# Kernel tuning notes

Measured on AMD Instinct MI355X. Metric: run time of the kernel, lower is better.

Reference implementation:

```python
import jax, jax.numpy as jnp
import numpy as np
import math

N_HEAD = 16

def setup_inputs() -> dict:
    key = jax.random.key(0)
    ks = jax.random.split(key, 5)
    B, T, C = 4, 2048, 1024
    x = jax.random.normal(ks[0], (B, T, C), dtype=jnp.float32)
    # xavier-uniform-ish scale for dense kernels
    W_attn = jax.random.normal(ks[1], (C, 3 * C), dtype=jnp.float32) * (1.0 / math.sqrt(C))
    b_attn = jnp.zeros((3 * C,), dtype=jnp.float32)
    W_proj = jax.random.normal(ks[2], (C, C), dtype=jnp.float32) * (1.0 / math.sqrt(C))
    b_proj = jnp.zeros((C,), dtype=jnp.float32)
    return {"x": x, "W_attn": W_attn, "b_attn": b_attn, "W_proj": W_proj, "b_proj": b_proj}

def reference(x, W_attn, b_attn, W_proj, b_proj):
    B, T, C = x.shape
    H = N_HEAD
    D = C // H
    qkv = x @ W_attn + b_attn                      # [B,T,3C]
    q, k, v = jnp.split(qkv, 3, axis=-1)
    q = q.reshape(B, T, H, D).transpose(0, 2, 1, 3)  # [B,H,T,D]
    k = k.reshape(B, T, H, D).transpose(0, 2, 1, 3)
    v = v.reshape(B, T, H, D).transpose(0, 2, 1, 3)
    att = jnp.einsum("bhqd,bhkd->bhqk", q, k) * (1.0 / math.sqrt(D))  # [B,H,T,T]
    causal = jnp.tril(jnp.ones((T, T), dtype=bool))
    att = jnp.where(causal, att, jnp.float32(-jnp.inf))
    att = jax.nn.softmax(att, axis=-1)             # exp(att - logsumexp)
    # dropout rates are 0.0 -> identity
    y = jnp.einsum("bhqk,bhkd->bhqd", att, v)      # [B,H,T,D]
    y = y.transpose(0, 2, 1, 3).reshape(B, T, C)
    y = y @ W_proj + b_proj
    return y
```

## Files before the change

kernel.cpp:

```cpp
#include <hip/hip_runtime.h>
#include <hip/hip_bf16.h>

typedef short s16x8 __attribute__((ext_vector_type(8)));
typedef float f32x4 __attribute__((ext_vector_type(4)));
typedef float f32x2 __attribute__((ext_vector_type(2)));

#define MFMA_BF16(A, B, C) __builtin_amdgcn_mfma_f32_16x16x32_bf16(A, B, C, 0, 0, 0)

constexpr int Bn = 4, Tn = 2048, Cn = 1024, Hn = 16, Dn = 64;
constexpr int Mn = Bn * Tn;
constexpr int Nqkv = 3 * Cn;
constexpr float SC = 0.125f * 1.44269504089f;

__device__ __forceinline__ ushort f2bfu(float f) {
    __hip_bfloat16 h = __float2bfloat16(f);
    return *reinterpret_cast<ushort*>(&h);
}
__device__ __forceinline__ uint pkbf(float a, float b) {
    __hip_bfloat162 h = __float22bfloat162_rn(make_float2(a, b));
    return *reinterpret_cast<uint*>(&h);
}

__device__ __forceinline__ f32x2 pk_add(f32x2 a, f32x2 b) {
    f32x2 d; asm("v_pk_add_f32 %0, %1, %2" : "=v"(d) : "v"(a), "v"(b)); return d;
}
__device__ __forceinline__ f32x2 pk_mul(f32x2 a, f32x2 b) {
    f32x2 d; asm("v_pk_mul_f32 %0, %1, %2" : "=v"(d) : "v"(a), "v"(b)); return d;
}

__device__ __forceinline__ void gl_lds16(const void* g, void* l) {
    __builtin_amdgcn_global_load_lds(
        (const __attribute__((address_space(1))) void*)(uintptr_t)g,
        (__attribute__((address_space(3))) void*)(uint32_t)(uintptr_t)l,
        16, 0, 0);
}

__global__ __launch_bounds__(256) void conv_bf16_kernel(
    const float* __restrict__ src, ushort* __restrict__ dst, int n4)
{
    int i = blockIdx.x * blockDim.x + threadIdx.x;
    int stride = gridDim.x * blockDim.x;
    for (; i < n4; i += stride) {
        float4 v = ((const float4*)src)[i];
        ushort4 o;
        o.x = f2bfu(v.x); o.y = f2bfu(v.y); o.z = f2bfu(v.z); o.w = f2bfu(v.w);
        ((ushort4*)dst)[i] = o;
    }
}

__global__ __launch_bounds__(256) void transpose_cvt_kernel(
    const float* __restrict__ W, ushort* __restrict__ Wt, int K, int N)
{
    __shared__ __align__(16) float Ls[64][68];
    const int t = threadIdx.x;
    const int n0 = blockIdx.x * 64, k0 = blockIdx.y * 64;
#pragma unroll
    for (int p = 0; p < 4; ++p) {
        int r = (t >> 4) + p * 16;
        int c = (t & 15) * 4;
        *(float4*)&Ls[r][c] = *(const float4*)&W[(size_t)(k0 + r) * N + n0 + c];
    }
    __syncthreads();
    const int n = t >> 2;
    const int ks = (t & 3) * 16;
    union { ushort s[16]; uint4 u[2]; } tmp;
#pragma unroll
    for (int j = 0; j < 16; ++j) tmp.s[j] = f2bfu(Ls[ks + j][n]);
    uint4* dp = (uint4*)&Wt[(size_t)(n0 + n) * K + k0 + ks];
    dp[0] = tmp.u[0];
    dp[1] = tmp.u[1];
}

__global__ __launch_bounds__(256) void vt_transpose_kernel(
    const ushort* __restrict__ V, ushort* __restrict__ Vt)
{
    const int tid = threadIdx.x;
    const int bh = blockIdx.x;
    const int kt0 = blockIdx.y * 64;
    const ushort* src = V + (size_t)bh * Tn * Dn;
    ushort* dst = Vt + (size_t)bh * Dn * Tn;
    const int vk = (tid & 15) * 4, vd = (tid >> 4) * 4;
    const ushort* g = src + (size_t)(kt0 + vk) * Dn + vd;
    ushort4 v0 = *(const ushort4*)(g);
    ushort4 v1 = *(const ushort4*)(g + Dn);
    ushort4 v2 = *(const ushort4*)(g + 2 * Dn);
    ushort4 v3 = *(const ushort4*)(g + 3 * Dn);
    ushort4 t0, t1, t2, t3;
    t0.x = v0.x; t0.y = v1.x; t0.z = v2.x; t0.w = v3.x;
    t1.x = v0.y; t1.y = v1.y; t1.z = v2.y; t1.w = v3.y;
    t2.x = v0.z; t2.y = v1.z; t2.z = v2.z; t2.w = v3.z;
    t3.x = v0.w; t3.y = v1.w; t3.z = v2.w; t3.w = v3.w;
    *(ushort4*)(dst + (size_t)(vd + 0) * Tn + kt0 + vk) = t0;
    *(ushort4*)(dst + (size_t)(vd + 1) * Tn + kt0 + vk) = t1;
    *(ushort4*)(dst + (size_t)(vd + 2) * Tn + kt0 + vk) = t2;
    *(ushort4*)(dst + (size_t)(vd + 3) * Tn + kt0 + vk) = t3;
}

__global__ __launch_bounds__(256) void qkv_gemm_mfma(
    const ushort* __restrict__ A, const ushort* __restrict__ Bt,
    const float* __restrict__ bias,
    ushort* __restrict__ Qo, ushort* __restrict__ Ko, ushort* __restrict__ Vo)
{
    __shared__ __align__(16) ushort As[128 * 64];
    __shared__ __align__(16) ushort Bs[128 * 64];
    const int tid = threadIdx.x;
    const int m0 = blockIdx.x * 128, n0 = blockIdx.y * 128;
    const int w = tid >> 6, lane = tid & 63, l15 = lane & 15, qd = lane >> 4;
    const int wm = (w >> 1) * 64, wn = (w & 1) * 64;
    const int lrow = lane >> 3;
    const int lchunk = (lane & 7) ^ (lrow & 7);

    const ushort* gA = A + (size_t)(m0 + w * 32 + lrow) * Cn + lchunk * 8;
    const ushort* gB = Bt + (size_t)(n0 + w * 32 + lrow) * Cn + lchunk * 8;
    ushort* lA = &As[(w * 32) * 64];
    ushort* lB = &Bs[(w * 32) * 64];

    f32x4 acc[4][4] = {};

    for (int k0 = 0; k0 < Cn; k0 += 64) {
        __syncthreads();
#pragma unroll
        for (int t = 0; t < 4; ++t) {
            gl_lds16(gA + (size_t)t * 8 * Cn + k0, lA + t * 8 * 64);
            gl_lds16(gB + (size_t)t * 8 * Cn + k0, lB + t * 8 * 64);
        }
        __syncthreads();
#pragma unroll
        for (int ks = 0; ks < 2; ++ks) {
            const int xs = (((ks * 4 + qd) ^ (l15 & 7))) * 8;
            s16x8 af[4], bfr[4];
#pragma unroll
            for (int i = 0; i < 4; ++i) {
                af[i]  = *(const s16x8*)&As[(wm + i * 16 + l15) * 64 + xs];
                bfr[i] = *(const s16x8*)&Bs[(wn + i * 16 + l15) * 64 + xs];
            }
#pragma unroll
            for (int mt = 0; mt < 4; ++mt)
#pragma unroll
                for (int nt = 0; nt < 4; ++nt)
                    acc[nt][mt] = MFMA_BF16(bfr[nt], af[mt], acc[nt][mt]);
        }
    }

#pragma unroll
    for (int nt = 0; nt < 4; ++nt) {
        const int n_b = n0 + wn + nt * 16 + qd * 4;
        const float4 bv = *(const float4*)&bias[n_b];
        const int sel = n_b >> 10;
        const int h = (n_b >> 6) & 15;
        const int d = n_b & 63;
        ushort* O = (sel == 0) ? Qo : ((sel == 1) ? Ko : Vo);
        const float scl = (sel == 0) ? SC : 1.0f;
#pragma unroll
        for (int mt = 0; mt < 4; ++mt) {
            const int m_g = m0 + wm + mt * 16 + l15;
            const int b = m_g >> 11, t = m_g & 2047;
            uint2 pk;
            pk.x = pkbf((acc[nt][mt][0] + bv.x) * scl,
                        (acc[nt][mt][1] + bv.y) * scl);
            pk.y = pkbf((acc[nt][mt][2] + bv.z) * scl,
                        (acc[nt][mt][3] + bv.w) * scl);
            *(uint2*)&O[(((size_t)(b * Hn + h) * Tn + t) << 6) + d] = pk;
        }
    }
}

__global__ __launch_bounds__(256, 4) void attn_mfma(
    const ushort* __restrict__ Q, const ushort* __restrict__ K,
    const ushort* __restrict__ Vt, ushort* __restrict__ Y)
{
    __shared__ __align__(16) ushort Ks[2][64 * 64];
    __shared__ __align__(16) ushort Vs[2][64 * 64];
    __shared__ __align__(16) ushort Ps[64 * 64];

    const int tid = threadIdx.x;
    const int bh = blockIdx.x, bx = blockIdx.y;
    const int w = tid >> 6, lane = tid & 63, l15 = lane & 15, qd = lane >> 4;
    const size_t base = (size_t)bh * Tn * Dn;
    const int lrow = lane >> 3;
    const int lchunk = (lane & 7) ^ (lrow & 7);
    const int q_l = w * 16 + l15;
    const int frow = q_l * 64;
    const int fx0 = ((0 * 4 + qd) ^ (l15 & 7)) * 8;
    const int fx1 = ((1 * 4 + qd) ^ (l15 & 7)) * 8;
    const int b = bh >> 4, h = bh & 15;

    const ushort* Kg = K + base + (size_t)(w * 16 + lrow) * Dn + lchunk * 8;
    const ushort* Vg = Vt + base + (size_t)(w * 16 + lrow) * Tn + lchunk * 8;
    const ushort* Qp = Q + base + (size_t)l15 * Dn + qd * 8;

#pragma unroll
    for (int half = 0; half < 2; ++half) {
        const int qt = half ? (31 - bx) : bx;

        const ushort* qrow = Qp + (size_t)(qt * 64 + w * 16) * Dn;
        s16x8 qf0 = *(const s16x8*)(qrow);
        s16x8 qf1 = *(const s16x8*)(qrow + 32);

        __syncthreads();
#pragma unroll
        for (int t = 0; t < 2; ++t) {
            gl_lds16(Kg + (size_t)(t * 8) * Dn, &Ks[0][(w * 16 + t * 8) * 64]);
            gl_lds16(Vg + (size_t)(t * 8) * Tn, &Vs[0][(w * 16 + t * 8) * 64]);
        }

        float m_run = -1e30f, l_run = 0.f;
        f32x4 o[4] = {};

        for (int kt = 0; kt <= qt; ++kt) {
            const int buf = kt & 1;
            __syncthreads();
            if (kt < qt) {
#pragma unroll
                for (int t = 0; t < 2; ++t) {
                    gl_lds16(Kg + (size_t)((kt + 1) * 64 + t * 8) * Dn,
                             &Ks[buf ^ 1][(w * 16 + t * 8) * 64]);
                    gl_lds16(Vg + (size_t)(t * 8) * Tn + (kt + 1) * 64,
                             &Vs[buf ^ 1][(w * 16 + t * 8) * 64]);
                }
            }

            f32x4 s[4] = {};
            __builtin_amdgcn_s_setprio(1);
#pragma unroll
            for (int nt = 0; nt < 4; ++nt) {
                s16x8 kf = *(const s16x8*)&Ks[buf][(nt * 16 + l15) * 64 + fx0];
                s[nt] = MFMA_BF16(kf, qf0, s[nt]);
            }
#pragma unroll
            for (int nt = 0; nt < 4; ++nt) {
                s16x8 kf = *(const s16x8*)&Ks[buf][(nt * 16 + l15) * 64 + fx1];
                s[nt] = MFMA_BF16(kf, qf1, s[nt]);
            }
            __builtin_amdgcn_s_setprio(0);

            if (kt == qt) {
#pragma unroll
                for (int nt = 0; nt < 4; ++nt)
#pragma unroll
                    for (int r = 0; r < 4; ++r)
                        if (nt * 16 + qd * 4 + r > q_l) s[nt][r] = -1e30f;
            }

            float a0 = fmaxf(fmaxf(s[0][0], s[0][1]), fmaxf(s[0][2], s[0][3]));
            float a1 = fmaxf(fmaxf(s[1][0], s[1][1]), fmaxf(s[1][2], s[1][3]));
            float a2 = fmaxf(fmaxf(s[2][0], s[2][1]), fmaxf(s[2][2], s[2][3]));
            float a3 = fmaxf(fmaxf(s[3][0], s[3][1]), fmaxf(s[3][2], s[3][3]));
            float mx = fmaxf(fmaxf(a0, a1), fmaxf(a2, a3));
            mx = fmaxf(mx, __shfl_xor(mx, 16));
            mx = fmaxf(mx, __shfl_xor(mx, 32));

            if (!__all(mx <= m_run + 8.f)) {
                float m_new = fmaxf(m_run, mx);
                float alpha = exp2f(m_run - m_new);
                m_run = m_new;
                l_run *= alpha;
                f32x2 aa = {alpha, alpha};
#pragma unroll
                for (int dt = 0; dt < 4; ++dt) {
                    o[dt].lo = pk_mul(o[dt].lo, aa);
                    o[dt].hi = pk_mul(o[dt].hi, aa);
                }
            }

            const f32x2 negm = {-m_run, -m_run};
            f32x2 lac0 = {0.f, 0.f}, lac1 = {0.f, 0.f};
#pragma unroll
            for (int nt = 0; nt < 4; ++nt) {
                s[nt].lo = pk_add(s[nt].lo, negm);
                s[nt].hi = pk_add(s[nt].hi, negm);
                s[nt][0] = exp2f(s[nt][0]);
                s[nt][1] = exp2f(s[nt][1]);
                s[nt][2] = exp2f(s[nt][2]);
                s[nt][3] = exp2f(s[nt][3]);
                lac0 = pk_add(lac0, s[nt].lo);
                lac1 = pk_add(lac1, s[nt].hi);
            }
            lac0 = pk_add(lac0, lac1);
            l_run += lac0[0] + lac0[1];

#pragma unroll
            for (int nt = 0; nt < 4; ++nt) {
                uint2 pk;
                pk.x = pkbf(s[nt][0], s[nt][1]);
                pk.y = pkbf(s[nt][2], s[nt][3]);
                const int pc = 2 * nt + (qd >> 1), po = (qd & 1) * 4;
                *(uint2*)&Ps[frow + ((pc ^ (l15 & 7)) * 8) + po] = pk;
            }

            {
                s16x8 pb = *(const s16x8*)&Ps[frow + fx0];
                __builtin_amdgcn_s_setprio(1);
#pragma unroll
                for (int dt = 0; dt < 4; ++dt) {
                    s16x8 vf = *(const s16x8*)&Vs[buf][(dt * 16 + l15) * 64 + fx0];
                    o[dt] = MFMA_BF16(vf, pb, o[dt]);
                }
                pb = *(const s16x8*)&Ps[frow + fx1];
#pragma unroll
                for (int dt = 0; dt < 4; ++dt) {
                    s16x8 vf = *(const s16x8*)&Vs[buf][(dt * 16 + l15) * 64 + fx1];
                    o[dt] = MFMA_BF16(vf, pb, o[dt]);
                }
                __builtin_amdgcn_s_setprio(0);
            }
        }

        float lt = l_run;
        lt += __shfl_xor(lt, 16);
        lt += __shfl_xor(lt, 32);
        const float inv = 1.f / lt;
        const int t_g = qt * 64 + w * 16 + l15;
        ushort* yp = Y + ((size_t)(b * Tn + t_g)) * Cn + h * Dn + qd * 4;
#pragma unroll
        for (int dt = 0; dt < 4; ++dt) {
            uint2 pk;
            pk.x = pkbf(o[dt][0] * inv, o[dt][1] * inv);
            pk.y = pkbf(o[dt][2] * inv, o[dt][3] * inv);
            *(uint2*)(yp + dt * 16) = pk;
        }
    }
}

__global__ __launch_bounds__(256) void proj_gemm_mfma(
    const ushort* __restrict__ A, const ushort* __restrict__ Bt,
    const float* __restrict__ bias, float* __restrict__ out)
{
    __shared__ __align__(16) ushort As[128 * 64];
    __shared__ __align__(16) ushort Bs[128 * 64];
    const int tid = threadIdx.x;
    const int m0 = blockIdx.x * 128, n0 = blockIdx.y * 128;
    const int w = tid >> 6, lane = tid & 63, l15 = lane & 15, qd = lane >> 4;
    const int wm = (w >> 1) * 64, wn = (w & 1) * 64;
    const int lrow = lane >> 3;
    const int lchunk = (lane & 7) ^ (lrow & 7);

    const ushort* gA = A + (size_t)(m0 + w * 32 + lrow) * Cn + lchunk * 8;
    const ushort* gB = Bt + (size_t)(n0 + w * 32 + lrow) * Cn + lchunk * 8;
    ushort* lA = &As[(w * 32) * 64];
    ushort* lB = &Bs[(w * 32) * 64];

    f32x4 acc[4][4] = {};

    for (int k0 = 0; k0 < Cn; k0 += 64) {
        __syncthreads();
#pragma unroll
        for (int t = 0; t < 4; ++t) {
            gl_lds16(gA + (size_t)t * 8 * Cn + k0, lA + t * 8 * 64);
            gl_lds16(gB + (size_t)t * 8 * Cn + k0, lB + t * 8 * 64);
        }
        __syncthreads();
#pragma unroll
        for (int ks = 0; ks < 2; ++ks) {
            const int xs = (((ks * 4 + qd) ^ (l15 & 7))) * 8;
            s16x8 af[4], bfr[4];
#pragma unroll
            for (int i = 0; i < 4; ++i) {
                af[i]  = *(const s16x8*)&As[(wm + i * 16 + l15) * 64 + xs];
                bfr[i] = *(const s16x8*)&Bs[(wn + i * 16 + l15) * 64 + xs];
            }
#pragma unroll
            for (int mt = 0; mt < 4; ++mt)
#pragma unroll
                for (int nt = 0; nt < 4; ++nt)
                    acc[mt][nt] = MFMA_BF16(af[mt], bfr[nt], acc[mt][nt]);
        }
    }

#pragma unroll
    for (int nt = 0; nt < 4; ++nt) {
        int n_g = n0 + wn + nt * 16 + l15;
        float bv = bias[n_g];
#pragma unroll
        for (int mt = 0; mt < 4; ++mt) {
#pragma unroll
            for (int r = 0; r < 4; ++r) {
                int m_g = m0 + wm + mt * 16 + qd * 4 + r;
                out[(size_t)m_g * Cn + n_g] = acc[mt][nt][r] + bv;
            }
        }
    }
}

extern "C" void kernel_launch(void* const* d_in, const int* in_sizes, int n_in,
                              void* d_out, int out_size, void* d_ws, size_t ws_size,
                              hipStream_t stream) {
    const float* x      = (const float*)d_in[0];
    const float* W_attn = (const float*)d_in[1];
    const float* b_attn = (const float*)d_in[2];
    const float* W_proj = (const float*)d_in[3];
    const float* b_proj = (const float*)d_in[4];
    float* out = (float*)d_out;

    constexpr size_t PER = (size_t)Mn * Cn;
    ushort* Qb = (ushort*)d_ws;
    ushort* Kb = Qb + PER;
    ushort* Vb = Kb + PER;
    ushort* Yb = Vb + PER;

    ushort* WtA  = (ushort*)d_out;
    ushort* x_bf = WtA + (size_t)Nqkv * Cn;
    ushort* Vtb  = (ushort*)d_out;
    ushort* WtP  = Qb;

    conv_bf16_kernel<<<1024, 256, 0, stream>>>(x, x_bf, (int)(PER / 4));
    transpose_cvt_kernel<<<dim3(Nqkv / 64, Cn / 64), 256, 0, stream>>>(
        W_attn, WtA, Cn, Nqkv);
    qkv_gemm_mfma<<<dim3(Mn / 128, Nqkv / 128), 256, 0, stream>>>(
        x_bf, WtA, b_attn, Qb, Kb, Vb);
    vt_transpose_kernel<<<dim3(Bn * Hn, Tn / 64), 256, 0, stream>>>(Vb, Vtb);
    attn_mfma<<<dim3(Bn * Hn, 16), 256, 0, stream>>>(Qb, Kb, Vtb, Yb);
    transpose_cvt_kernel<<<dim3(Cn / 64, Cn / 64), 256, 0, stream>>>(
        W_proj, WtP, Cn, Cn);
    proj_gemm_mfma<<<dim3(Mn / 128, Cn / 128), 256, 0, stream>>>(
        Yb, WtP, b_proj, out);
}
```

Measured before the change: 273.4 us.

## Fuse V transpose into QKV GEMM epilogue and drop separate transpose kernel

The QKV GEMM now branches per block: blocks producing V write their results directly in the transposed [B,H,D,T] layout that attention consumes. This removes the standalone vt_transpose kernel and its extra read and write pass over V. The Q/K path also swaps the MFMA operand order so that its epilogue writes scalar bf16 stores across the head dimension instead of packed uint2 stores. The V buffer moves into workspace instead of aliasing the output. The trade-off is more, narrower 2-byte stores in the GEMM epilogue, which may cost store efficiency.

```diff
diff --git a/kernel.cpp b/kernel.cpp
--- a/kernel.cpp
+++ b/kernel.cpp
@@ -69,31 +69,6 @@
     uint4* dp = (uint4*)&Wt[(size_t)(n0 + n) * K + k0 + ks];
     dp[0] = tmp.u[0];
     dp[1] = tmp.u[1];
-}
-
-__global__ __launch_bounds__(256) void vt_transpose_kernel(
-    const ushort* __restrict__ V, ushort* __restrict__ Vt)
-{
-    const int tid = threadIdx.x;
-    const int bh = blockIdx.x;
-    const int kt0 = blockIdx.y * 64;
-    const ushort* src = V + (size_t)bh * Tn * Dn;
-    ushort* dst = Vt + (size_t)bh * Dn * Tn;
-    const int vk = (tid & 15) * 4, vd = (tid >> 4) * 4;
-    const ushort* g = src + (size_t)(kt0 + vk) * Dn + vd;
-    ushort4 v0 = *(const ushort4*)(g);
-    ushort4 v1 = *(const ushort4*)(g + Dn);
-    ushort4 v2 = *(const ushort4*)(g + 2 * Dn);
-    ushort4 v3 = *(const ushort4*)(g + 3 * Dn);
-    ushort4 t0, t1, t2, t3;
-    t0.x = v0.x; t0.y = v1.x; t0.z = v2.x; t0.w = v3.x;
-    t1.x = v0.y; t1.y = v1.y; t1.z = v2.y; t1.w = v3.y;
-    t2.x = v0.z; t2.y = v1.z; t2.z = v2.z; t2.w = v3.z;
-    t3.x = v0.w; t3.y = v1.w; t3.z = v2.w; t3.w = v3.w;
-    *(ushort4*)(dst + (size_t)(vd + 0) * Tn + kt0 + vk) = t0;
-    *(ushort4*)(dst + (size_t)(vd + 1) * Tn + kt0 + vk) = t1;
-    *(ushort4*)(dst + (size_t)(vd + 2) * Tn + kt0 + vk) = t2;
-    *(ushort4*)(dst + (size_t)(vd + 3) * Tn + kt0 + vk) = t3;
 }
 
 __global__ __launch_bounds__(256) void qkv_gemm_mfma(
@@ -116,51 +91,94 @@
     ushort* lB = &Bs[(w * 32) * 64];
 
     f32x4 acc[4][4] = {};
-
-    for (int k0 = 0; k0 < Cn; k0 += 64) {
-        __syncthreads();
-#pragma unroll
-        for (int t = 0; t < 4; ++t) {
-            gl_lds16(gA + (size_t)t * 8 * Cn + k0, lA + t * 8 * 64);
-            gl_lds16(gB + (size_t)t * 8 * Cn + k0, lB + t * 8 * 64);
-        }
-        __syncthreads();
-#pragma unroll
-        for (int ks = 0; ks < 2; ++ks) {
-            const int xs = (((ks * 4 + qd) ^ (l15 & 7))) * 8;
-            s16x8 af[4], bfr[4];
-#pragma unroll
-            for (int i = 0; i < 4; ++i) {
-                af[i]  = *(const s16x8*)&As[(wm + i * 16 + l15) * 64 + xs];
-                bfr[i] = *(const s16x8*)&Bs[(wn + i * 16 + l15) * 64 + xs];
-            }
-#pragma unroll
-            for (int mt = 0; mt < 4; ++mt)
-#pragma unroll
-                for (int nt = 0; nt < 4; ++nt)
-                    acc[nt][mt] = MFMA_BF16(bfr[nt], af[mt], acc[nt][mt]);
-        }
-    }
-
-#pragma unroll
-    for (int nt = 0; nt < 4; ++nt) {
-        const int n_b = n0 + wn + nt * 16 + qd * 4;
-        const float4 bv = *(const float4*)&bias[n_b];
-        const int sel = n_b >> 10;
-        const int h = (n_b >> 6) & 15;
-        const int d = n_b & 63;
-        ushort* O = (sel == 0) ? Qo : ((sel == 1) ? Ko : Vo);
+    const bool isV = (n0 >= 2 * Cn);
+
+    if (!isV) {
+        for (int k0 = 0; k0 < Cn; k0 += 64) {
+            __syncthreads();
+#pragma unroll
+            for (int t = 0; t < 4; ++t) {
+                gl_lds16(gA + (size_t)t * 8 * Cn + k0, lA + t * 8 * 64);
+                gl_lds16(gB + (size_t)t * 8 * Cn + k0, lB + t * 8 * 64);
+            }
+            __syncthreads();
+#pragma unroll
+            for (int ks = 0; ks < 2; ++ks) {
+                const int xs = (((ks * 4 + qd) ^ (l15 & 7))) * 8;
+                s16x8 af[4], bfr[4];
+#pragma unroll
+                for (int i = 0; i < 4; ++i) {
+                    af[i]  = *(const s16x8*)&As[(wm + i * 16 + l15) * 64 + xs];
+                    bfr[i] = *(const s16x8*)&Bs[(wn + i * 16 + l15) * 64 + xs];
+                }
+#pragma unroll
+                for (int mt = 0; mt < 4; ++mt)
+#pragma unroll
+                    for (int nt = 0; nt < 4; ++nt)
+                        acc[mt][nt] = MFMA_BF16(af[mt], bfr[nt], acc[mt][nt]);
+            }
+        }
+        const int sel = n0 >> 10;
+        ushort* O = (sel == 0) ? Qo : Ko;
         const float scl = (sel == 0) ? SC : 1.0f;
 #pragma unroll
-        for (int mt = 0; mt < 4; ++mt) {
-            const int m_g = m0 + wm + mt * 16 + l15;
-            const int b = m_g >> 11, t = m_g & 2047;
-            uint2 pk;
-            pk.x = pkbf((acc[nt][mt][0] + bv.x) * scl,
-                        (acc[nt][mt][1] + bv.y) * scl);
-            pk.y = pkbf((acc[nt][mt][2] + bv.z) * scl,
-                        (acc[nt][mt][3] + bv.w) * scl);
-            *(uint2*)&O[(((size_t)(b * Hn + h) * Tn + t) << 6) + d] = pk;
+        for (int nt = 0; nt < 4; ++nt) {
+            const int n_g = n0 + wn + nt * 16 + l15;
+            const float bv = bias[n_g];
+            const int h = (n_g >> 6) & 15;
+            const int d = n_g & 63;
+#pragma unroll
+            for (int mt = 0; mt < 4; ++mt) {
+#pragma unroll
+                for (int r = 0; r < 4; ++r) {
+                    const int m_g = m0 + wm + mt * 16 + qd * 4 + r;
+                    const int b = m_g >> 11, t = m_g & 2047;
+                    O[(((size_t)(b * Hn + h) * Tn + t) << 6) + d] =
+                        f2bfu((acc[mt][nt][r] + bv) * scl);
+                }
+            }
+        }
+    } else {
+        for (int k0 = 0; k0 < Cn; k0 += 64) {
+            __syncthreads();
+#pragma unroll
+            for (int t = 0; t < 4; ++t) {
+                gl_lds16(gA + (size_t)t * 8 * Cn + k0, lA + t * 8 * 64);
+                gl_lds16(gB + (size_t)t * 8 * Cn + k0, lB + t * 8 * 64);
+            }
+            __syncthreads();
+#pragma unroll
+            for (int ks = 0; ks < 2; ++ks) {
+                const int xs = (((ks * 4 + qd) ^ (l15 & 7))) * 8;
+                s16x8 af[4], bfr[4];
+#pragma unroll
+                for (int i = 0; i < 4; ++i) {
+                    af[i]  = *(const s16x8*)&As[(wm + i * 16 + l15) * 64 + xs];
+                    bfr[i] = *(const s16x8*)&Bs[(wn + i * 16 + l15) * 64 + xs];
+                }
+#pragma unroll
+                for (int mt = 0; mt < 4; ++mt)
+#pragma unroll
+                    for (int nt = 0; nt < 4; ++nt)
+                        acc[nt][mt] = MFMA_BF16(bfr[nt], af[mt], acc[nt][mt]);
+            }
+        }
+#pragma unroll
+        for (int nt = 0; nt < 4; ++nt) {
+            const int n_b = n0 + wn + nt * 16 + qd * 4;
+            const float4 bv = *(const float4*)&bias[n_b];
+            const int h = (n_b >> 6) & 15;
+            const int d0 = n_b & 63;
+#pragma unroll
+            for (int mt = 0; mt < 4; ++mt) {
+                const int m_g = m0 + wm + mt * 16 + l15;
+                const int b = m_g >> 11, tt = m_g & 2047;
+                const size_t rowb = (size_t)(b * Hn + h) * Dn;
+                Vo[(rowb + d0 + 0) * Tn + tt] = f2bfu(acc[nt][mt][0] + bv.x);
+                Vo[(rowb + d0 + 1) * Tn + tt] = f2bfu(acc[nt][mt][1] + bv.y);
+                Vo[(rowb + d0 + 2) * Tn + tt] = f2bfu(acc[nt][mt][2] + bv.z);
+                Vo[(rowb + d0 + 3) * Tn + tt] = f2bfu(acc[nt][mt][3] + bv.w);
+            }
         }
     }
 }
@@ -393,22 +411,20 @@
     float* out = (float*)d_out;
 
     constexpr size_t PER = (size_t)Mn * Cn;
-    ushort* Qb = (ushort*)d_ws;
-    ushort* Kb = Qb + PER;
-    ushort* Vb = Kb + PER;
-    ushort* Yb = Vb + PER;
+    ushort* Qb  = (ushort*)d_ws;
+    ushort* Kb  = Qb + PER;
+    ushort* Vtb = Kb + PER;
+    ushort* Yb  = Vtb + PER;
 
     ushort* WtA  = (ushort*)d_out;
     ushort* x_bf = WtA + (size_t)Nqkv * Cn;
-    ushort* Vtb  = (ushort*)d_out;
     ushort* WtP  = Qb;
 
     conv_bf16_kernel<<<1024, 256, 0, stream>>>(x, x_bf, (int)(PER / 4));
     transpose_cvt_kernel<<<dim3(Nqkv / 64, Cn / 64), 256, 0, stream>>>(
         W_attn, WtA, Cn, Nqkv);
     qkv_gemm_mfma<<<dim3(Mn / 128, Nqkv / 128), 256, 0, stream>>>(
-        x_bf, WtA, b_attn, Qb, Kb, Vb);
-    vt_transpose_kernel<<<dim3(Bn * Hn, Tn / 64), 256, 0, stream>>>(Vb, Vtb);
+        x_bf, WtA, b_attn, Qb, Kb, Vtb);
     attn_mfma<<<dim3(Bn * Hn, 16), 256, 0, stream>>>(Qb, Kb, Vtb, Yb);
     transpose_cvt_kernel<<<dim3(Cn / 64, Cn / 64), 256, 0, stream>>>(
         W_proj, WtP, Cn, Cn);
```

New measurement: 254.1 us. -7.0%, faster.
